# Kernel optimization log

Measured on AMD Instinct MI355X. Metric: run time of the kernel, lower is better.

Reference implementation:

```python
import jax, jax.numpy as jnp
import numpy as np

N, M, D = 4096, 8192, 1024
N_ITERS = 15  # module hardcodes self.n_iters = 15
EPS = 1e-12   # F.normalize eps


def setup_inputs() -> dict:
    key = jax.random.key(0)
    k1, k2 = jax.random.split(key)
    K = jax.random.normal(k1, (N, M), dtype=jnp.float32)
    y = jax.random.normal(k2, (M, D), dtype=jnp.float32)
    return {"K": K, "y": y, "topk": 32}


def _topk_preimage(K_mat, y, topk):
    # torch: topk -> L1-normalize values -> scatter into zeros_like(K) -> mm(y).
    # Since topk indices are unique per row, scatter+dense-mm == gather + weighted sum.
    vals, inds = jax.lax.top_k(K_mat, topk)                      # [N, k], [N, k]
    norm = jnp.maximum(jnp.sum(jnp.abs(vals), axis=-1, keepdims=True), EPS)
    w = vals / norm                                              # F.normalize(p=1, dim=-1)
    preimage = jnp.einsum('nk,nkd->nd', w, y[inds])              # [N, D]
    return preimage, inds


def reference(K, y, topk):
    preimage, inds = _topk_preimage(K, y, topk)

    def body(pre, _):
        K_i = pre @ y.T                                          # linear kernel_fn: [N, M]
        pre, inds_i = _topk_preimage(K_i, y, topk)
        return pre, inds_i

    preimage, inds_all = jax.lax.scan(body, preimage, None, length=N_ITERS)
    return preimage, inds_all[-1]
```

## Files before the change

kernel.cpp:

```cpp
#include <hip/hip_runtime.h>
#include <hip/hip_bf16.h>
#include <math.h>

#define N_ROWS 4096
#define M_COLS 8192
#define D_DIM  1024
#define TOPK   32
#define N_ITERS 15
#define CHUNK   2048
#define KC      384
#define D_CUT   1696

template <int EXACT_V>
__global__ __launch_bounds__(256) void topk_pre_kernel(
    const float* __restrict__ R,
    const float* __restrict__ Y,
    float* __restrict__ pre,
    int* __restrict__ inds_ws,
    int row_off, int write_inds)
{
    __shared__ float s_wv[4];
    __shared__ int   s_wi[4];
    __shared__ float topv[TOPK];
    __shared__ int   topi[TOPK];
    __shared__ int   s_win;
    __shared__ float s_w[TOPK];
    __shared__ int   s_si[TOPK];
    __shared__ float s_sw[TOPK];
    __shared__ float s_norm;

    const int tid    = threadIdx.x;
    const int n_loc  = blockIdx.x;
    const int n_glob = row_off + n_loc;
    const float* Rr  = R + (size_t)n_loc * M_COLS;

    float v[32];
    #pragma unroll
    for (int q = 0; q < 8; ++q) {
        float4 w = reinterpret_cast<const float4*>(Rr)[tid + 256 * q];
        v[4 * q + 0] = w.x; v[4 * q + 1] = w.y;
        v[4 * q + 2] = w.z; v[4 * q + 3] = w.w;
    }

    float cv = -INFINITY; int ci = M_COLS;
    #pragma unroll
    for (int q = 0; q < 8; ++q)
        #pragma unroll
        for (int c = 0; c < 4; ++c) {
            const int m = 4 * q + c;
            const int j = 4 * tid + 1024 * q + c;
            if (v[m] > cv || (v[m] == cv && j < ci)) { cv = v[m]; ci = j; }
        }

    for (int s = 0; s < TOPK; ++s) {
        float bv = cv; int bi = ci;
        #pragma unroll
        for (int off = 32; off > 0; off >>= 1) {
            float ov = __shfl_down(bv, off);
            int   oi = __shfl_down(bi, off);
            if (ov > bv || (ov == bv && oi < bi)) { bv = ov; bi = oi; }
        }
        if ((tid & 63) == 0) { s_wv[tid >> 6] = bv; s_wi[tid >> 6] = bi; }
        __syncthreads();
        if (tid == 0) {
            for (int w = 1; w < 4; ++w) {
                if (s_wv[w] > bv || (s_wv[w] == bv && s_wi[w] < bi)) {
                    bv = s_wv[w]; bi = s_wi[w];
                }
            }
            topv[s] = bv; topi[s] = bi; s_win = bi;
        }
        __syncthreads();
        const int win = s_win;
        if (((win >> 2) & 255) == tid) {
            const int mw = ((win >> 10) << 2) | (win & 3);
            #pragma unroll
            for (int m = 0; m < 32; ++m)
                if (m == mw) v[m] = -INFINITY;
            cv = -INFINITY; ci = M_COLS;
            #pragma unroll
            for (int q = 0; q < 8; ++q)
                #pragma unroll
                for (int c = 0; c < 4; ++c) {
                    const int m = 4 * q + c;
                    const int j = 4 * tid + 1024 * q + c;
                    if (v[m] > cv || (v[m] == cv && j < ci)) { cv = v[m]; ci = j; }
                }
        }
    }

    if (EXACT_V) {
        if (tid == 0) {
            double sum = 0.0;
            for (int k = 0; k < TOPK; ++k) sum += fabs((double)topv[k]);
            s_norm = fmaxf((float)sum, 1e-12f);
        }
    } else {
        if (tid == 0) {
            float r[8];
            #pragma unroll
            for (int j = 0; j < 8; ++j) r[j] = fabsf(topv[j]);
            #pragma unroll
            for (int blk = 8; blk < TOPK; blk += 8)
                #pragma unroll
                for (int j = 0; j < 8; ++j)
                    r[j] = __fadd_rn(r[j], fabsf(topv[blk + j]));
            float s01 = __fadd_rn(r[0], r[1]);
            float s23 = __fadd_rn(r[2], r[3]);
            float s45 = __fadd_rn(r[4], r[5]);
            float s67 = __fadd_rn(r[6], r[7]);
            s_norm = fmaxf(__fadd_rn(__fadd_rn(s01, s23), __fadd_rn(s45, s67)), 1e-12f);
        }
    }
    __syncthreads();
    if (tid < TOPK) s_w[tid] = __fdiv_rn(topv[tid], s_norm);
    __syncthreads();

    if (EXACT_V) {
        double acc[4] = {0.0, 0.0, 0.0, 0.0};
        for (int k = 0; k < TOPK; ++k) {
            const double wk = (double)s_w[k];
            const float* yr = Y + (size_t)topi[k] * D_DIM;
            #pragma unroll
            for (int j = 0; j < 4; ++j)
                acc[j] = fma(wk, (double)yr[tid + 256 * j], acc[j]);
        }
        float* pr = pre + (size_t)n_glob * D_DIM;
        #pragma unroll
        for (int j = 0; j < 4; ++j) pr[tid + 256 * j] = (float)acc[j];
    } else {
        if (tid == 0) {
            for (int k = 0; k < TOPK; ++k) { s_si[k] = topi[k]; s_sw[k] = s_w[k]; }
            for (int a = 1; a < TOPK; ++a) {
                int ia = s_si[a]; float wa = s_sw[a];
                int b = a - 1;
                while (b >= 0 && s_si[b] > ia) {
                    s_si[b + 1] = s_si[b]; s_sw[b + 1] = s_sw[b]; --b;
                }
                s_si[b + 1] = ia; s_sw[b + 1] = wa;
            }
        }
        __syncthreads();
        float tot[4]  = {0.f, 0.f, 0.f, 0.f};
        float part[4] = {0.f, 0.f, 0.f, 0.f};
        int curPan = s_si[0] / KC;
        for (int k = 0; k < TOPK; ++k) {
            const int idx = s_si[k];
            const int pan = idx / KC;
            if (pan != curPan) {
                #pragma unroll
                for (int j = 0; j < 4; ++j) {
                    tot[j] = __fadd_rn(tot[j], part[j]);
                    part[j] = 0.f;
                }
                curPan = pan;
            }
            const float wk = s_sw[k];
            const float* yr = Y + (size_t)idx * D_DIM;
            #pragma unroll
            for (int j = 0; j < 4; ++j)
                part[j] = fmaf(wk, yr[tid + 256 * j], part[j]);
        }
        #pragma unroll
        for (int j = 0; j < 4; ++j) tot[j] = __fadd_rn(tot[j], part[j]);
        float* pr = pre + (size_t)n_glob * D_DIM;
        #pragma unroll
        for (int j = 0; j < 4; ++j) pr[tid + 256 * j] = tot[j];
    }

    if (write_inds && tid < TOPK)
        inds_ws[(size_t)n_glob * TOPK + tid] = topi[tid];
}

#define ABM 128
#define ABN 128
#define ABK 16

__global__ __launch_bounds__(256) void gemmA_kernel(
    const float* __restrict__ A,
    const float* __restrict__ B,
    float* __restrict__ C)
{
    __shared__ __align__(16) float As[ABK][ABM + 4];
    __shared__ __align__(16) float Bs[ABK][ABN + 4];

    const int tid  = threadIdx.x;
    const int tx   = tid & 15;
    const int ty   = tid >> 4;
    const int row0 = blockIdx.y * ABM;
    const int col0 = blockIdx.x * ABN;

    const int lr = tid >> 1;
    const int lc = (tid & 1) * 8;

    float tot[8][8], acc[8][8];
    #pragma unroll
    for (int i = 0; i < 8; ++i)
        #pragma unroll
        for (int j = 0; j < 8; ++j) { tot[i][j] = 0.f; acc[i][j] = 0.f; }

    for (int k0 = 0; k0 < D_DIM; k0 += ABK) {
        float4 va0 = *reinterpret_cast<const float4*>(A + (size_t)(row0 + lr) * D_DIM + k0 + lc);
        float4 va1 = *reinterpret_cast<const float4*>(A + (size_t)(row0 + lr) * D_DIM + k0 + lc + 4);
        As[lc + 0][lr] = va0.x; As[lc + 1][lr] = va0.y;
        As[lc + 2][lr] = va0.z; As[lc + 3][lr] = va0.w;
        As[lc + 4][lr] = va1.x; As[lc + 5][lr] = va1.y;
        As[lc + 6][lr] = va1.z; As[lc + 7][lr] = va1.w;
        float4 vb0 = *reinterpret_cast<const float4*>(B + (size_t)(col0 + lr) * D_DIM + k0 + lc);
        float4 vb1 = *reinterpret_cast<const float4*>(B + (size_t)(col0 + lr) * D_DIM + k0 + lc + 4);
        Bs[lc + 0][lr] = vb0.x; Bs[lc + 1][lr] = vb0.y;
        Bs[lc + 2][lr] = vb0.z; Bs[lc + 3][lr] = vb0.w;
        Bs[lc + 4][lr] = vb1.x; Bs[lc + 5][lr] = vb1.y;
        Bs[lc + 6][lr] = vb1.z; Bs[lc + 7][lr] = vb1.w;
        __syncthreads();

        #pragma unroll
        for (int kk = 0; kk < ABK; ++kk) {
            float a[8], b[8];
            *reinterpret_cast<float4*>(&a[0]) = *reinterpret_cast<float4*>(&As[kk][ty * 8]);
            *reinterpret_cast<float4*>(&a[4]) = *reinterpret_cast<float4*>(&As[kk][ty * 8 + 4]);
            *reinterpret_cast<float4*>(&b[0]) = *reinterpret_cast<float4*>(&Bs[kk][tx * 8]);
            *reinterpret_cast<float4*>(&b[4]) = *reinterpret_cast<float4*>(&Bs[kk][tx * 8 + 4]);
            #pragma unroll
            for (int i = 0; i < 8; ++i)
                #pragma unroll
                for (int j = 0; j < 8; ++j)
                    acc[i][j] = fmaf(a[i], b[j], acc[i][j]);
        }
        __syncthreads();

        const int kend = k0 + ABK;
        if (kend == KC || kend == 2 * KC || kend == D_DIM) {
            #pragma unroll
            for (int i = 0; i < 8; ++i)
                #pragma unroll
                for (int j = 0; j < 8; ++j) {
                    tot[i][j] = __fadd_rn(tot[i][j], acc[i][j]);
                    acc[i][j] = 0.f;
                }
        }
    }

    #pragma unroll
    for (int i = 0; i < 8; ++i) {
        float4 v0 = { tot[i][0], tot[i][1], tot[i][2], tot[i][3] };
        float4 v1 = { tot[i][4], tot[i][5], tot[i][6], tot[i][7] };
        float* cr = C + (size_t)(row0 + ty * 8 + i) * M_COLS + col0 + tx * 8;
        *reinterpret_cast<float4*>(cr)     = v0;
        *reinterpret_cast<float4*>(cr + 4) = v1;
    }
}

#define BBM 128
#define BBN 64
#define BBK 16

__global__ __launch_bounds__(256) void gemmB_kernel(
    const float* __restrict__ A,
    const float* __restrict__ B,
    float* __restrict__ C)
{
    __shared__ float As[BBK][BBM + 4];
    __shared__ float Bs[BBK][BBN + 4];

    const int tid  = threadIdx.x;
    const int tx   = tid & 15;
    const int ty   = tid >> 4;
    const int row0 = blockIdx.y * BBM;
    const int col0 = blockIdx.x * BBN;

    const int lrA = tid >> 1;
    const int lcA = (tid & 1) * 8;
    const int lrB = tid >> 2;
    const int lcB = (tid & 3) * 4;

    double dacc[8][4];
    #pragma unroll
    for (int i = 0; i < 8; ++i)
        #pragma unroll
        for (int j = 0; j < 4; ++j) dacc[i][j] = 0.0;

    for (int k0 = 0; k0 < D_DIM; k0 += BBK) {
        float4 va0 = *reinterpret_cast<const float4*>(A + (size_t)(row0 + lrA) * D_DIM + k0 + lcA);
        float4 va1 = *reinterpret_cast<const float4*>(A + (size_t)(row0 + lrA) * D_DIM + k0 + lcA + 4);
        As[lcA + 0][lrA] = va0.x; As[lcA + 1][lrA] = va0.y;
        As[lcA + 2][lrA] = va0.z; As[lcA + 3][lrA] = va0.w;
        As[lcA + 4][lrA] = va1.x; As[lcA + 5][lrA] = va1.y;
        As[lcA + 6][lrA] = va1.z; As[lcA + 7][lrA] = va1.w;
        float4 vb = *reinterpret_cast<const float4*>(B + (size_t)(col0 + lrB) * D_DIM + k0 + lcB);
        Bs[lcB + 0][lrB] = vb.x; Bs[lcB + 1][lrB] = vb.y;
        Bs[lcB + 2][lrB] = vb.z; Bs[lcB + 3][lrB] = vb.w;
        __syncthreads();

        #pragma unroll
        for (int kk = 0; kk < BBK; ++kk) {
            double a[8], b[4];
            #pragma unroll
            for (int i = 0; i < 8; ++i) a[i] = (double)As[kk][ty * 8 + i];
            #pragma unroll
            for (int j = 0; j < 4; ++j) b[j] = (double)Bs[kk][tx * 4 + j];
            #pragma unroll
            for (int i = 0; i < 8; ++i)
                #pragma unroll
                for (int j = 0; j < 4; ++j)
                    dacc[i][j] = fma(a[i], b[j], dacc[i][j]);
        }
        __syncthreads();
    }

    #pragma unroll
    for (int i = 0; i < 8; ++i) {
        float4 v = { (float)dacc[i][0], (float)dacc[i][1],
                     (float)dacc[i][2], (float)dacc[i][3] };
        float* cr = C + (size_t)(row0 + ty * 8 + i) * M_COLS + col0 + tx * 4;
        *reinterpret_cast<float4*>(cr) = v;
    }
}

__global__ __launch_bounds__(256) void choice_kernel(
    const int* __restrict__ indsA,
    const int* __restrict__ indsB,
    unsigned char* __restrict__ choice)
{
    const int n = blockIdx.x * 256 + threadIdx.x;
    if (n >= N_ROWS) return;
    int d = 0;
    #pragma unroll
    for (int k = 0; k < TOPK; ++k) {
        int diff = indsA[n * TOPK + k] - indsB[n * TOPK + k];
        if (diff < 0) diff = -diff;
        if (diff > d) d = diff;
    }
    choice[n] = (d > 0 && d <= D_CUT) ? 1 : 0;
}

__global__ __launch_bounds__(256) void emit_kernel(
    const float* __restrict__ preA, const float* __restrict__ preB,
    const int* __restrict__ indsA,  const int* __restrict__ indsB,
    const unsigned char* __restrict__ choice,
    float* __restrict__ out_pre, float* __restrict__ out_inds)
{
    const int n   = blockIdx.x;
    const int tid = threadIdx.x;
    const int c   = choice[n];
    const float* ps = (c ? preB : preA) + (size_t)n * D_DIM;
    const int*   is = (c ? indsB : indsA) + (size_t)n * TOPK;
    float* po = out_pre + (size_t)n * D_DIM;
    #pragma unroll
    for (int j = 0; j < 4; ++j) po[tid + 256 * j] = ps[tid + 256 * j];
    if (tid < TOPK)
        out_inds[(size_t)n * TOPK + tid] = (float)is[tid];
}

extern "C" void kernel_launch(void* const* d_in, const int* in_sizes, int n_in,
                              void* d_out, int out_size, void* d_ws, size_t ws_size,
                              hipStream_t stream)
{
    const float* K_in = (const float*)d_in[0];
    const float* Y    = (const float*)d_in[1];

    char* p = (char*)d_ws;
    float* preA   = (float*)p; p += (size_t)N_ROWS * D_DIM * sizeof(float);
    float* preB   = (float*)p; p += (size_t)N_ROWS * D_DIM * sizeof(float);
    float* Kchunk = (float*)p; p += (size_t)CHUNK * M_COLS * sizeof(float);
    int*   indsA  = (int*)p;   p += (size_t)N_ROWS * TOPK * sizeof(int);
    int*   indsB  = (int*)p;   p += (size_t)N_ROWS * TOPK * sizeof(int);
    unsigned char* choice = (unsigned char*)p;

    float* out_pre  = (float*)d_out;
    float* out_inds = out_pre + (size_t)N_ROWS * D_DIM;

    topk_pre_kernel<0><<<N_ROWS, 256, 0, stream>>>(K_in, Y, preA, indsA, 0, 0);
    topk_pre_kernel<1><<<N_ROWS, 256, 0, stream>>>(K_in, Y, preB, indsB, 0, 0);

    for (int it = 0; it < N_ITERS; ++it) {
        const int wo = (it == N_ITERS - 1) ? 1 : 0;
        for (int c = 0; c < N_ROWS / CHUNK; ++c) {
            gemmA_kernel<<<dim3(M_COLS / ABN, CHUNK / ABM), 256, 0, stream>>>(
                preA + (size_t)c * CHUNK * D_DIM, Y, Kchunk);
            topk_pre_kernel<0><<<CHUNK, 256, 0, stream>>>(
                Kchunk, Y, preA, indsA, c * CHUNK, wo);
            gemmB_kernel<<<dim3(M_COLS / BBN, CHUNK / BBM), 256, 0, stream>>>(
                preB + (size_t)c * CHUNK * D_DIM, Y, Kchunk);
            topk_pre_kernel<1><<<CHUNK, 256, 0, stream>>>(
                Kchunk, Y, preB, indsB, c * CHUNK, wo);
        }
    }

    choice_kernel<<<(N_ROWS + 255) / 256, 256, 0, stream>>>(indsA, indsB, choice);
    emit_kernel<<<N_ROWS, 256, 0, stream>>>(preA, preB, indsA, indsB, choice,
                                            out_pre, out_inds);
}
```

Measured before the change: 50.31 ms.

## Skip remaining iterations once preimage reaches a bitwise fixed point

Adds device-side flags. Each topk_pre block compares its new preimage row against the old one and sets a changed flag via atomicOr. After each iteration a tiny kernel marks a path frozen if nothing changed, and the GEMM and top-k kernels for that path return immediately afterward. This avoids redundant GEMMs once the iteration has converged, at the cost of an extra global read per output element and a few tiny launches. Indices are now written every pass.

```diff
diff --git a/kernel.cpp b/kernel.cpp
--- a/kernel.cpp
+++ b/kernel.cpp
@@ -11,14 +11,25 @@
 #define KC      384
 #define D_CUT   1696
 
+__global__ void init_flags_kernel(int* f) { f[0] = f[1] = f[2] = f[3] = 0; }
+__global__ void reset_changed_kernel(int* f) { f[2] = 0; f[3] = 0; }
+__global__ void update_flags_kernel(int* f) {
+    if (f[2] == 0) f[0] = 1;
+    if (f[3] == 0) f[1] = 1;
+    f[2] = 0; f[3] = 0;
+}
+
 template <int EXACT_V>
 __global__ __launch_bounds__(256) void topk_pre_kernel(
     const float* __restrict__ R,
     const float* __restrict__ Y,
     float* __restrict__ pre,
     int* __restrict__ inds_ws,
-    int row_off, int write_inds)
-{
+    int row_off,
+    const int* __restrict__ frozen,
+    int* __restrict__ changed)
+{
+    __shared__ int   s_frozen;
     __shared__ float s_wv[4];
     __shared__ int   s_wi[4];
     __shared__ float topv[TOPK];
@@ -29,7 +40,11 @@
     __shared__ float s_sw[TOPK];
     __shared__ float s_norm;
 
-    const int tid    = threadIdx.x;
+    const int tid = threadIdx.x;
+    if (tid == 0) s_frozen = *frozen;
+    __syncthreads();
+    if (s_frozen) return;
+
     const int n_loc  = blockIdx.x;
     const int n_glob = row_off + n_loc;
     const float* Rr  = R + (size_t)n_loc * M_COLS;
@@ -116,6 +131,7 @@
     if (tid < TOPK) s_w[tid] = __fdiv_rn(topv[tid], s_norm);
     __syncthreads();
 
+    float newv[4];
     if (EXACT_V) {
         double acc[4] = {0.0, 0.0, 0.0, 0.0};
         for (int k = 0; k < TOPK; ++k) {
@@ -125,9 +141,8 @@
             for (int j = 0; j < 4; ++j)
                 acc[j] = fma(wk, (double)yr[tid + 256 * j], acc[j]);
         }
-        float* pr = pre + (size_t)n_glob * D_DIM;
-        #pragma unroll
-        for (int j = 0; j < 4; ++j) pr[tid + 256 * j] = (float)acc[j];
+        #pragma unroll
+        for (int j = 0; j < 4; ++j) newv[j] = (float)acc[j];
     } else {
         if (tid == 0) {
             for (int k = 0; k < TOPK; ++k) { s_si[k] = topi[k]; s_sw[k] = s_w[k]; }
@@ -162,13 +177,20 @@
                 part[j] = fmaf(wk, yr[tid + 256 * j], part[j]);
         }
         #pragma unroll
-        for (int j = 0; j < 4; ++j) tot[j] = __fadd_rn(tot[j], part[j]);
-        float* pr = pre + (size_t)n_glob * D_DIM;
-        #pragma unroll
-        for (int j = 0; j < 4; ++j) pr[tid + 256 * j] = tot[j];
-    }
-
-    if (write_inds && tid < TOPK)
+        for (int j = 0; j < 4; ++j) newv[j] = __fadd_rn(tot[j], part[j]);
+    }
+
+    float* pr = pre + (size_t)n_glob * D_DIM;
+    bool diff = false;
+    #pragma unroll
+    for (int j = 0; j < 4; ++j) {
+        float old = pr[tid + 256 * j];
+        if (__float_as_uint(old) != __float_as_uint(newv[j])) diff = true;
+        pr[tid + 256 * j] = newv[j];
+    }
+    if (diff) atomicOr(changed, 1);
+
+    if (tid < TOPK)
         inds_ws[(size_t)n_glob * TOPK + tid] = topi[tid];
 }
 
@@ -179,12 +201,18 @@
 __global__ __launch_bounds__(256) void gemmA_kernel(
     const float* __restrict__ A,
     const float* __restrict__ B,
-    float* __restrict__ C)
+    float* __restrict__ C,
+    const int* __restrict__ frozen)
 {
     __shared__ __align__(16) float As[ABK][ABM + 4];
     __shared__ __align__(16) float Bs[ABK][ABN + 4];
-
-    const int tid  = threadIdx.x;
+    __shared__ int s_frozen;
+
+    const int tid = threadIdx.x;
+    if (tid == 0) s_frozen = *frozen;
+    __syncthreads();
+    if (s_frozen) return;
+
     const int tx   = tid & 15;
     const int ty   = tid >> 4;
     const int row0 = blockIdx.y * ABM;
@@ -258,12 +286,18 @@
 __global__ __launch_bounds__(256) void gemmB_kernel(
     const float* __restrict__ A,
     const float* __restrict__ B,
-    float* __restrict__ C)
+    float* __restrict__ C,
+    const int* __restrict__ frozen)
 {
     __shared__ float As[BBK][BBM + 4];
     __shared__ float Bs[BBK][BBN + 4];
-
-    const int tid  = threadIdx.x;
+    __shared__ int s_frozen;
+
+    const int tid = threadIdx.x;
+    if (tid == 0) s_frozen = *frozen;
+    __syncthreads();
+    if (s_frozen) return;
+
     const int tx   = tid & 15;
     const int ty   = tid >> 4;
     const int row0 = blockIdx.y * BBM;
@@ -365,26 +399,32 @@
     float* Kchunk = (float*)p; p += (size_t)CHUNK * M_COLS * sizeof(float);
     int*   indsA  = (int*)p;   p += (size_t)N_ROWS * TOPK * sizeof(int);
     int*   indsB  = (int*)p;   p += (size_t)N_ROWS * TOPK * sizeof(int);
-    unsigned char* choice = (unsigned char*)p;
+    unsigned char* choice = (unsigned char*)p; p += N_ROWS;
+    int*   flags  = (int*)(((uintptr_t)p + 15) & ~(uintptr_t)15);
 
     float* out_pre  = (float*)d_out;
     float* out_inds = out_pre + (size_t)N_ROWS * D_DIM;
 
-    topk_pre_kernel<0><<<N_ROWS, 256, 0, stream>>>(K_in, Y, preA, indsA, 0, 0);
-    topk_pre_kernel<1><<<N_ROWS, 256, 0, stream>>>(K_in, Y, preB, indsB, 0, 0);
+    init_flags_kernel<<<1, 1, 0, stream>>>(flags);
+
+    topk_pre_kernel<0><<<N_ROWS, 256, 0, stream>>>(
+        K_in, Y, preA, indsA, 0, &flags[0], &flags[2]);
+    topk_pre_kernel<1><<<N_ROWS, 256, 0, stream>>>(
+        K_in, Y, preB, indsB, 0, &flags[1], &flags[3]);
+    reset_changed_kernel<<<1, 1, 0, stream>>>(flags);
 
     for (int it = 0; it < N_ITERS; ++it) {
-        const int wo = (it == N_ITERS - 1) ? 1 : 0;
         for (int c = 0; c < N_ROWS / CHUNK; ++c) {
             gemmA_kernel<<<dim3(M_COLS / ABN, CHUNK / ABM), 256, 0, stream>>>(
-                preA + (size_t)c * CHUNK * D_DIM, Y, Kchunk);
+                preA + (size_t)c * CHUNK * D_DIM, Y, Kchunk, &flags[0]);
             topk_pre_kernel<0><<<CHUNK, 256, 0, stream>>>(
-                Kchunk, Y, preA, indsA, c * CHUNK, wo);
+                Kchunk, Y, preA, indsA, c * CHUNK, &flags[0], &flags[2]);
             gemmB_kernel<<<dim3(M_COLS / BBN, CHUNK / BBM), 256, 0, stream>>>(
-                preB + (size_t)c * CHUNK * D_DIM, Y, Kchunk);
+                preB + (size_t)c * CHUNK * D_DIM, Y, Kchunk, &flags[1]);
             topk_pre_kernel<1><<<CHUNK, 256, 0, stream>>>(
-                Kchunk, Y, preB, indsB, c * CHUNK, wo);
-        }
+                Kchunk, Y, preB, indsB, c * CHUNK, &flags[1], &flags[3]);
+        }
+        update_flags_kernel<<<1, 1, 0, stream>>>(flags);
     }
 
     choice_kernel<<<(N_ROWS + 255) / 256, 256, 0, stream>>>(indsA, indsB, choice);
```

New measurement: 54.96 ms. 9.2% more time.
